# Kernel tuning notes

Measured on AMD Instinct MI355X. Metric: run time of the kernel, lower is better.

Reference implementation:

```python
import math
import jax, jax.numpy as jnp
import numpy as np

IN_DIM = 1024
OUT_DIM = 1024
K = 32
N_BANDS = 3
TOTAL_K = K * N_BANDS
LAYER_IDX = 0
NUM_LAYERS = 1
SCALE = math.sqrt(2.0 / (IN_DIM + OUT_DIM))


def _make_pos():
    l_val = (LAYER_IDX + 1) / (NUM_LAYERS + 1)
    i_idx = (jnp.arange(IN_DIM, dtype=jnp.float32) + 1) / (IN_DIM + 1)
    j_idx = (jnp.arange(OUT_DIM, dtype=jnp.float32) + 1) / (OUT_DIM + 1)
    ii, jj = jnp.meshgrid(i_idx, j_idx, indexing='ij')
    pos = jnp.stack([ii, jj, jnp.full_like(ii, l_val)], axis=-1)
    return pos.reshape(-1, 3)  # (in_dim*out_dim, 3)


def setup_inputs() -> dict:
    key = jax.random.key(0)
    kx, ko, kp, ka = jax.random.split(key, 4)
    x = jax.random.normal(kx, (4096, IN_DIM), dtype=jnp.float32)
    # omega with per-band scaling (1 + band*3), matching the torch init
    band_scales = jnp.repeat(1.0 + 3.0 * jnp.arange(N_BANDS, dtype=jnp.float32), K)
    omega = jax.random.normal(ko, (TOTAL_K, 3), dtype=jnp.float32) * band_scales[:, None]
    phi = jax.random.normal(kp, (TOTAL_K,), dtype=jnp.float32) * math.pi
    alpha = jax.random.normal(ka, (2 * TOTAL_K,), dtype=jnp.float32) * 0.01 / (1.0 + jnp.arange(2 * TOTAL_K, dtype=jnp.float32))
    bias = jnp.zeros((OUT_DIM,), dtype=jnp.float32)
    pos = _make_pos()
    return {"x": x, "omega": omega, "phi": phi, "alpha": alpha, "bias": bias, "pos": pos}


def reference(x, omega, phi, alpha, bias, pos):
    # args: (in*out, total_k)
    args = pos @ omega.T + phi
    # features @ alpha == sin(args)@alpha[:K2//2] + cos(args)@alpha[K2//2:]
    a_sin, a_cos = alpha[:TOTAL_K], alpha[TOTAL_K:]
    w_flat = jnp.sin(args) @ a_sin + jnp.cos(args) @ a_cos  # (in*out,)
    # torch: w = flat.reshape(in, out).T * scale; F.linear(x, w) = x @ w.T
    w_t = w_flat.reshape(IN_DIM, OUT_DIM) * SCALE  # == w.T
    return x @ w_t + bias
```

## Files before the change

kernel.cpp:

```cpp
#include <hip/hip_runtime.h>
#include <hip/hip_bf16.h>
#include <math.h>


#define IN_DIM   1024
#define OUT_DIM  1024
#define NBANDS   96
#define KTAB     192
#define MX       4096
#define SCALE_W  0.03125f

typedef __bf16 bf16x8 __attribute__((ext_vector_type(8)));
typedef float  f32x4  __attribute__((ext_vector_type(4)));

#define AS1 __attribute__((address_space(1)))
#define AS3 __attribute__((address_space(3)))

__device__ __forceinline__ void gload_lds16(const void* g, void* l) {
  __builtin_amdgcn_global_load_lds((AS1 void*)(g), (AS3 void*)(l), 16, 0, 0);
}

__device__ __forceinline__ unsigned short bf16bits(float f) {
  __hip_bfloat16 b = __float2bfloat16(f);
  return *(unsigned short*)&b;
}

__global__ void build_tables(const float* __restrict__ omega,
                             const float* __restrict__ phi,
                             const float* __restrict__ alpha,
                             __hip_bfloat16* __restrict__ TaT,
                             __hip_bfloat16* __restrict__ Tb) {
  const int t = blockIdx.x;
  const int i = blockIdx.y * 256 + threadIdx.x;
  const float ox = omega[3 * t], oy = omega[3 * t + 1], oz = omega[3 * t + 2];
  const float uc = oz * 0.5f + phi[t];
  const float as_ = alpha[t], ac = alpha[NBANDS + t];
  const float coord = (float)(i + 1) / 1025.0f;
  float su, cu;
  sincosf(ox * coord + uc, &su, &cu);
  TaT[(size_t)(2 * t) * IN_DIM + i]     = __float2bfloat16(SCALE_W * (as_ * su + ac * cu));
  TaT[(size_t)(2 * t + 1) * IN_DIM + i] = __float2bfloat16(SCALE_W * (as_ * cu - ac * su));
  float sv, cv;
  sincosf(oy * coord, &sv, &cv);
  Tb[(size_t)i * KTAB + 2 * t]     = __float2bfloat16(cv);
  Tb[(size_t)i * KTAB + 2 * t + 1] = __float2bfloat16(sv);
}

__global__ __launch_bounds__(256)
void gemm_xta(const float* __restrict__ X,
              const __hip_bfloat16* __restrict__ TaT,
              __hip_bfloat16* __restrict__ Y) {
  __shared__ __align__(16) __hip_bfloat16 As[2][16 * 64];
  __shared__ __align__(16) __hip_bfloat16 Bs[2][192 * 64];
  const int tid  = threadIdx.x;
  const int lane = tid & 63;
  const int wc   = tid >> 6;
  const int m0   = blockIdx.x * 16;
  const int lr = lane & 15;
  const int hi = lane >> 4;

  const float* xbase = X + (size_t)m0 * IN_DIM;

  f32x4 acc[3] = {};

  auto ALOAD = [&](int t, float4& a) {
    const int r = tid >> 4, c4 = tid & 15;
    a = *(const float4*)(xbase + (size_t)r * IN_DIM + t * 64 + c4 * 4);
  };
  auto AWRITE = [&](int buf, const float4& a) {
    const int r = tid >> 4, c4 = tid & 15;
    ushort4 o;
    o.x = bf16bits(a.x); o.y = bf16bits(a.y);
    o.z = bf16bits(a.z); o.w = bf16bits(a.w);
    const int byte = r * 128 + ((((c4 >> 1) ^ (r & 7)) << 4) | ((c4 & 1) << 3));
    *(ushort4*)((char*)&As[buf][0] + byte) = o;
  };
  auto BSTAGE = [&](int t, int buf) {
#pragma unroll
    for (int q = 0; q < 6; ++q) {
      const int f = q * 256 + tid;
      const int r = f >> 3, g = f & 7;
      gload_lds16(TaT + (size_t)r * IN_DIM + t * 64 + ((g ^ (r & 7)) * 8),
                  (char*)&Bs[buf][0] + (size_t)f * 16);
    }
  };
  auto COMPUTE = [&](int buf) {
#pragma unroll
    for (int kk = 0; kk < 2; ++kk) {
      bf16x8 af, bfr[3];
      af = *(const bf16x8*)((char*)&As[buf][0] +
            lr * 128 + (((kk * 4 + hi) ^ (lr & 7)) << 4));
#pragma unroll
      for (int ni = 0; ni < 3; ++ni) {
        const int row = wc * 48 + ni * 16 + lr;
        bfr[ni] = *(const bf16x8*)((char*)&Bs[buf][0] +
                   row * 128 + (((kk * 4 + hi) ^ (row & 7)) << 4));
      }
#pragma unroll
      for (int ni = 0; ni < 3; ++ni)
        acc[ni] = __builtin_amdgcn_mfma_f32_16x16x32_bf16(
            af, bfr[ni], acc[ni], 0, 0, 0);
    }
  };

  float4 a0;
  ALOAD(0, a0); BSTAGE(0, 0); AWRITE(0, a0);
  __syncthreads();
#pragma unroll
  for (int t = 0; t < 16; ++t) {
    const int cur = t & 1;
    float4 an;
    if (t < 15) { ALOAD(t + 1, an); BSTAGE(t + 1, cur ^ 1); }
    COMPUTE(cur);
    if (t < 15) AWRITE(cur ^ 1, an);
    __syncthreads();
  }

#pragma unroll
  for (int ni = 0; ni < 3; ++ni)
#pragma unroll
    for (int r = 0; r < 4; ++r) {
      const int row = m0 + hi * 4 + r;
      const int col = wc * 48 + ni * 16 + lr;
      Y[(size_t)row * KTAB + col] = __float2bfloat16(acc[ni][r]);
    }
}

__global__ __launch_bounds__(256)
void gemm_out(const __hip_bfloat16* __restrict__ Y,
              const __hip_bfloat16* __restrict__ Tb,
              float* __restrict__ out,
              const float* __restrict__ bias) {
  __shared__ __align__(16) __hip_bfloat16 As[2][64 * 64];
  __shared__ __align__(16) __hip_bfloat16 Bs[2][128 * 64];
  const int tid  = threadIdx.x;
  const int lane = tid & 63;
  const int wave = tid >> 6;
  const int wr = wave >> 1;
  const int wc = wave & 1;
  const int m0 = blockIdx.y * 64;
  const int n0 = blockIdx.x * 128;
  const int lr = lane & 15;
  const int hi = lane >> 4;

  f32x4 acc[2][4] = {};

  auto ASTAGE = [&](int t, int buf) {
#pragma unroll
    for (int q = 0; q < 2; ++q) {
      const int f = q * 256 + tid;
      const int r = f >> 3, g = f & 7;
      gload_lds16(Y + (size_t)(m0 + r) * KTAB + t * 64 + ((g ^ (r & 7)) * 8),
                  (char*)&As[buf][0] + (size_t)f * 16);
    }
  };
  auto BSTAGE = [&](int t, int buf) {
#pragma unroll
    for (int q = 0; q < 4; ++q) {
      const int f = q * 256 + tid;
      const int r = f >> 3, g = f & 7;
      gload_lds16(Tb + (size_t)(n0 + r) * KTAB + t * 64 + ((g ^ (r & 7)) * 8),
                  (char*)&Bs[buf][0] + (size_t)f * 16);
    }
  };
  auto COMPUTE = [&](int buf) {
#pragma unroll
    for (int kk = 0; kk < 2; ++kk) {
      bf16x8 af[2], bfr[4];
#pragma unroll
      for (int mi = 0; mi < 2; ++mi) {
        const int row = wr * 32 + mi * 16 + lr;
        af[mi] = *(const bf16x8*)((char*)&As[buf][0] +
                  row * 128 + (((kk * 4 + hi) ^ (row & 7)) << 4));
      }
#pragma unroll
      for (int ni = 0; ni < 4; ++ni) {
        const int row = wc * 64 + ni * 16 + lr;
        bfr[ni] = *(const bf16x8*)((char*)&Bs[buf][0] +
                   row * 128 + (((kk * 4 + hi) ^ (row & 7)) << 4));
      }
#pragma unroll
      for (int mi = 0; mi < 2; ++mi)
#pragma unroll
        for (int ni = 0; ni < 4; ++ni)
          acc[mi][ni] = __builtin_amdgcn_mfma_f32_16x16x32_bf16(
              af[mi], bfr[ni], acc[mi][ni], 0, 0, 0);
    }
  };

  ASTAGE(0, 0); BSTAGE(0, 0);
  __syncthreads();
#pragma unroll
  for (int t = 0; t < 3; ++t) {
    const int cur = t & 1;
    if (t < 2) { ASTAGE(t + 1, cur ^ 1); BSTAGE(t + 1, cur ^ 1); }
    COMPUTE(cur);
    __syncthreads();
  }

#pragma unroll
  for (int mi = 0; mi < 2; ++mi)
#pragma unroll
    for (int ni = 0; ni < 4; ++ni)
#pragma unroll
      for (int r = 0; r < 4; ++r) {
        const int row = m0 + wr * 32 + mi * 16 + hi * 4 + r;
        const int col = n0 + wc * 64 + ni * 16 + lr;
        out[(size_t)row * OUT_DIM + col] = acc[mi][ni][r] + bias[col];
      }
}

extern "C" void kernel_launch(void* const* d_in, const int* in_sizes, int n_in,
                              void* d_out, int out_size, void* d_ws, size_t ws_size,
                              hipStream_t stream) {
  const float* x     = (const float*)d_in[0];
  const float* omega = (const float*)d_in[1];
  const float* phi   = (const float*)d_in[2];
  const float* alpha = (const float*)d_in[3];
  const float* bias  = (const float*)d_in[4];
  float* out = (float*)d_out;
  (void)in_sizes; (void)n_in; (void)out_size; (void)ws_size;

  char* ws = (char*)d_ws;
  __hip_bfloat16* Y   = (__hip_bfloat16*)(ws);
  __hip_bfloat16* TaT = (__hip_bfloat16*)(ws + 1572864);
  __hip_bfloat16* Tb  = (__hip_bfloat16*)(ws + 1966080);

  build_tables<<<dim3(NBANDS, 4), dim3(256), 0, stream>>>(omega, phi, alpha, TaT, Tb);
  gemm_xta<<<dim3(MX / 16), dim3(256), 0, stream>>>(x, TaT, Y);
  gemm_out<<<dim3(OUT_DIM / 128, MX / 64), dim3(256), 0, stream>>>(Y, Tb, out, bias);
}
```

Baseline: 100.8 us.

## Use partial vmcnt waits and deepen X prefetch in both GEMM kernels

```diff
diff --git a/kernel.cpp b/kernel.cpp
--- a/kernel.cpp
+++ b/kernel.cpp
@@ -23,6 +23,18 @@
 __device__ __forceinline__ unsigned short bf16bits(float f) {
   __hip_bfloat16 b = __float2bfloat16(f);
   return *(unsigned short*)&b;
+}
+
+__device__ __forceinline__ void wait_vm_lgkm(int n) {
+  switch (n) {
+    case 7: asm volatile("s_waitcnt vmcnt(7) lgkmcnt(0)" ::: "memory"); break;
+    case 6: asm volatile("s_waitcnt vmcnt(6) lgkmcnt(0)" ::: "memory"); break;
+    default: asm volatile("s_waitcnt vmcnt(0) lgkmcnt(0)" ::: "memory"); break;
+  }
+}
+__device__ __forceinline__ void lgkm0_barrier() {
+  asm volatile("s_waitcnt lgkmcnt(0)" ::: "memory");
+  __builtin_amdgcn_s_barrier();
 }
 
 __global__ void build_tables(const float* __restrict__ omega,
@@ -103,17 +115,22 @@
     }
   };
 
-  float4 a0;
-  ALOAD(0, a0); BSTAGE(0, 0); AWRITE(0, a0);
-  __syncthreads();
+  float4 areg[2];
+  ALOAD(0, areg[0]);
+  BSTAGE(0, 0);
+  ALOAD(1, areg[1]);
+  AWRITE(0, areg[0]);
+
 #pragma unroll
   for (int t = 0; t < 16; ++t) {
     const int cur = t & 1;
-    float4 an;
-    if (t < 15) { ALOAD(t + 1, an); BSTAGE(t + 1, cur ^ 1); }
+    if (t < 15) BSTAGE(t + 1, cur ^ 1);
+    if (t < 14) ALOAD(t + 2, areg[t & 1]);
+    wait_vm_lgkm(t < 14 ? 7 : (t < 15 ? 6 : 0));
+    __builtin_amdgcn_s_barrier();
     COMPUTE(cur);
-    if (t < 15) AWRITE(cur ^ 1, an);
-    __syncthreads();
+    if (t < 15) AWRITE(cur ^ 1, areg[(t + 1) & 1]);
+    lgkm0_barrier();
   }
 
 #pragma unroll
@@ -189,13 +206,14 @@
   };
 
   ASTAGE(0, 0); BSTAGE(0, 0);
-  __syncthreads();
 #pragma unroll
   for (int t = 0; t < 3; ++t) {
     const int cur = t & 1;
     if (t < 2) { ASTAGE(t + 1, cur ^ 1); BSTAGE(t + 1, cur ^ 1); }
+    wait_vm_lgkm(t < 2 ? 6 : 0);
+    __builtin_amdgcn_s_barrier();
     COMPUTE(cur);
-    __syncthreads();
+    lgkm0_barrier();
   }
 
 #pragma unroll
```

Measured after the change: 99.62 us. About the same (-1.2%).
